# Kernel optimization log

Measured on AMD Instinct MI355X. Metric: run time of the kernel, lower is better.

Reference implementation:

```python
import jax, jax.numpy as jnp
import numpy as np

DIM = 768
NUM_HEADS = 12
HEAD_DIM = DIM // NUM_HEADS
EPS = 1e-6  # flax nn.LayerNorm default


def layer_norm(x, scale, bias):
    # LayerNorm over last axis (head_dim)
    mean = jnp.mean(x, axis=-1, keepdims=True)
    var = jnp.var(x, axis=-1, keepdims=True)
    return (x - mean) * jax.lax.rsqrt(var + EPS) * scale + bias


def setup_inputs() -> dict:
    key = jax.random.key(0)
    k0, = jax.random.split(key, 1)
    B, N = 4, 2048
    QKV = jax.random.normal(k0, (B, N, 3 * DIM), dtype=jnp.float32)
    return {
        "QKV": QKV,
        "q_scale": jnp.ones((HEAD_DIM,), jnp.float32),
        "q_bias": jnp.zeros((HEAD_DIM,), jnp.float32),
        "k_scale": jnp.ones((HEAD_DIM,), jnp.float32),
        "k_bias": jnp.zeros((HEAD_DIM,), jnp.float32),
    }


def reference(QKV, q_scale, q_bias, k_scale, k_bias):
    B, N, C = QKV.shape
    qkv = QKV.reshape(B, N, 3, NUM_HEADS, HEAD_DIM)
    qkv = jnp.transpose(qkv, (2, 0, 3, 1, 4))  # [3, B, H, N, d]
    q, k, v = qkv[0], qkv[1], qkv[2]
    q = layer_norm(q, q_scale, q_bias)
    k = layer_norm(k, k_scale, k_bias)
    attn = jnp.einsum('bhqd,bhkd->bhqk', q, k) * (HEAD_DIM ** -0.5)
    attn = jax.nn.softmax(attn, axis=-1)
    x = jnp.einsum('bhqk,bhkd->bhqd', attn, v)
    return x
```

## Files before the change

### kernel.cpp

```cpp
#include <hip/hip_runtime.h>
#include <math.h>

#define NB   4
#define SEQ  2048
#define NH   12
#define CIN  2304
#define TM   64
#define NCH  (SEQ/TM)
#define TQ   128

typedef _Float16 half8 __attribute__((ext_vector_type(8)));
typedef _Float16 half4 __attribute__((ext_vector_type(4)));
typedef float    f32x4 __attribute__((ext_vector_type(4)));
typedef unsigned int u32;
#define AS1 __attribute__((address_space(1)))
#define AS3 __attribute__((address_space(3)))

#define TILE_B  8192
#define KT_BYTES ((size_t)NB*NH*NCH*TILE_B)
#define WS_FULL  (2*KT_BYTES)

static __device__ __forceinline__ int dec_xcd(int id, int& b, int& h, int& q0) {
    const int xcd = id & 7;
    const int qt  = (id >> 3) & 15;
    const int grp = id >> 7;
    const int bh  = grp * 8 + xcd;
    b = bh / NH; h = bh - b * NH; q0 = qt * TQ;
    return bh;
}

__global__ __launch_bounds__(256, 4)
void preprocess_kernel(const float* __restrict__ QKV,
                       const float* __restrict__ k_scale,
                       const float* __restrict__ k_bias,
                       unsigned char* __restrict__ ws, int writeV)
{
    const int tid = threadIdx.x;
    const int L   = tid & 63;
    const int wv  = tid >> 6;
    const int r4  = L >> 2;
    const int c4  = L & 3;
    const int mc  = blockIdx.x, h = blockIdx.y, b = blockIdx.z;

    unsigned char* Kt = ws + (size_t)((b*NH + h)*NCH + mc) * TILE_B;

    const float4* QKV4 = (const float4*)QKV;
    const int row = wv*16 + r4;
    const size_t base4 = (size_t)(b*SEQ + mc*64 + row) * 576 + h*16 + c4*4;

    {
        float4 x[4];
        #pragma unroll
        for (int i = 0; i < 4; ++i) x[i] = QKV4[base4 + 192 + i];
        float s = 0.f, s2 = 0.f;
        #pragma unroll
        for (int i = 0; i < 4; ++i) {
            s  += x[i].x + x[i].y + x[i].z + x[i].w;
            s2 += x[i].x*x[i].x + x[i].y*x[i].y + x[i].z*x[i].z + x[i].w*x[i].w;
        }
        s  += __shfl_xor(s, 1);  s  += __shfl_xor(s, 2);
        s2 += __shfl_xor(s2, 1); s2 += __shfl_xor(s2, 2);
        float mu = s * 0.015625f;
        float rstd = rsqrtf(s2 * 0.015625f - mu*mu + 1e-6f);
        float nb0 = -mu * rstd;
        half8 h0, h1;
        #pragma unroll
        for (int i = 0; i < 4; ++i) {
            float4 sc = ((const float4*)k_scale)[c4*4 + i];
            float4 bi = ((const float4*)k_bias)[c4*4 + i];
            float e0 = fmaf(x[i].x, rstd, nb0) * sc.x + bi.x;
            float e1 = fmaf(x[i].y, rstd, nb0) * sc.y + bi.y;
            float e2 = fmaf(x[i].z, rstd, nb0) * sc.z + bi.z;
            float e3 = fmaf(x[i].w, rstd, nb0) * sc.w + bi.w;
            if (i < 2) { h0[i*4+0]=(_Float16)e0; h0[i*4+1]=(_Float16)e1; h0[i*4+2]=(_Float16)e2; h0[i*4+3]=(_Float16)e3; }
            else { int j=(i-2)*4; h1[j+0]=(_Float16)e0; h1[j+1]=(_Float16)e1; h1[j+2]=(_Float16)e2; h1[j+3]=(_Float16)e3; }
        }
        *(half8*)(Kt + row*128 + (((2*c4+0) ^ (row & 7)) * 16)) = h0;
        *(half8*)(Kt + row*128 + (((2*c4+1) ^ (row & 7)) * 16)) = h1;
    }

    if (writeV) {
        unsigned char* Vt = ws + KT_BYTES + (size_t)((b*NH + h)*NCH + mc) * TILE_B;
        const float* gv = QKV + (size_t)(b*SEQ + mc*64 + wv*16)*CIN + 1536 + h*64 + L;
        float vvp[16];
        #pragma unroll
        for (int j = 0; j < 16; ++j) vvp[j] = gv[(size_t)j * CIN];
        half8 a0, a1;
        #pragma unroll
        for (int j = 0; j < 8; ++j) { a0[j] = (_Float16)vvp[j]; a1[j] = (_Float16)vvp[j+8]; }
        *(half8*)(Vt + L*128 + (((2*wv+0) ^ (L & 7)) * 16)) = a0;
        *(half8*)(Vt + L*128 + (((2*wv+1) ^ (L & 7)) * 16)) = a1;
    }
}

#define Q_PROLOGUE(QTBASE)                                                        \
    const float SC = 0.125f * 1.44269504088896340736f;                            \
    _Pragma("unroll")                                                             \
    for (int g = 0; g < 2; ++g) {                                                 \
        const int row = wv*32 + g*16 + r4;                                        \
        const size_t base4 = (size_t)(b*SEQ + q0 + row) * 576 + h*16 + c4*4;      \
        float4 x[4];                                                              \
        _Pragma("unroll")                                                         \
        for (int i = 0; i < 4; ++i) x[i] = QKV4[base4 + i];                       \
        float s = 0.f, s2 = 0.f;                                                  \
        _Pragma("unroll")                                                         \
        for (int i = 0; i < 4; ++i) {                                             \
            s  += x[i].x + x[i].y + x[i].z + x[i].w;                              \
            s2 += x[i].x*x[i].x + x[i].y*x[i].y + x[i].z*x[i].z + x[i].w*x[i].w;  \
        }                                                                         \
        s  += __shfl_xor(s, 1);  s  += __shfl_xor(s, 2);                          \
        s2 += __shfl_xor(s2, 1); s2 += __shfl_xor(s2, 2);                         \
        float mu = s * 0.015625f;                                                 \
        float rstd = rsqrtf(s2 * 0.015625f - mu*mu + 1e-6f);                      \
        float nb0 = -mu * rstd;                                                   \
        half8 h0, h1;                                                             \
        _Pragma("unroll")                                                         \
        for (int i = 0; i < 4; ++i) {                                             \
            float4 sc = ((const float4*)q_scale)[c4*4 + i];                       \
            float4 bi = ((const float4*)q_bias)[c4*4 + i];                        \
            float e0 = (fmaf(x[i].x, rstd, nb0) * sc.x + bi.x) * SC;              \
            float e1 = (fmaf(x[i].y, rstd, nb0) * sc.y + bi.y) * SC;              \
            float e2 = (fmaf(x[i].z, rstd, nb0) * sc.z + bi.z) * SC;              \
            float e3 = (fmaf(x[i].w, rstd, nb0) * sc.w + bi.w) * SC;              \
            if (i < 2) { h0[i*4+0]=(_Float16)e0; h0[i*4+1]=(_Float16)e1; h0[i*4+2]=(_Float16)e2; h0[i*4+3]=(_Float16)e3; } \
            else { int j=(i-2)*4; h1[j+0]=(_Float16)e0; h1[j+1]=(_Float16)e1; h1[j+2]=(_Float16)e2; h1[j+3]=(_Float16)e3; } \
        }                                                                         \
        *(half8*)((QTBASE) + row*128 + (((2*c4+0) ^ (r4 & 7)) * 16)) = h0;        \
        *(half8*)((QTBASE) + row*128 + (((2*c4+1) ^ (r4 & 7)) * 16)) = h1;        \
    }                                                                             \
    half8 qf[2][2];                                                               \
    _Pragma("unroll")                                                             \
    for (int s = 0; s < 2; ++s) {                                                 \
        const unsigned char* qrow = (QTBASE) + (wv*32 + s*16 + n16)*128;          \
        _Pragma("unroll")                                                         \
        for (int ks = 0; ks < 2; ++ks)                                            \
            qf[s][ks] = *(const half8*)(qrow + (((quad + 4*ks) ^ sw) * 16));      \
    }

#define CHUNK_COMPUTE(KAB, VTB)                                                   \
    {                                                                             \
        f32x4 sacc[2][4] = {};                                                    \
        _Pragma("unroll")                                                         \
        for (int ks = 0; ks < 2; ++ks) {                                          \
            half8 ak[4];                                                          \
            _Pragma("unroll")                                                     \
            for (int mt = 0; mt < 4; ++mt)                                        \
                ak[mt] = *(const half8*)((KAB) + (16*mt + n16)*128 + (((quad + 4*ks) ^ sw) * 16)); \
            _Pragma("unroll")                                                     \
            for (int s = 0; s < 2; ++s)                                           \
                _Pragma("unroll")                                                 \
                for (int mt = 0; mt < 4; ++mt)                                    \
                    sacc[s][mt] = __builtin_amdgcn_mfma_f32_16x16x32_f16(ak[mt], qf[s][ks], sacc[s][mt], 0, 0, 0); \
        }                                                                         \
        _Pragma("unroll")                                                         \
        for (int s = 0; s < 2; ++s) {                                             \
            float ls = 0.f;                                                       \
            _Pragma("unroll")                                                     \
            for (int mt = 0; mt < 4; ++mt) {                                      \
                float p0 = __builtin_exp2f(sacc[s][mt][0]);                       \
                float p1 = __builtin_exp2f(sacc[s][mt][1]);                       \
                float p2 = __builtin_exp2f(sacc[s][mt][2]);                       \
                float p3 = __builtin_exp2f(sacc[s][mt][3]);                       \
                ls += (p0 + p1) + (p2 + p3);                                      \
                half4 hp; hp[0]=(_Float16)p0; hp[1]=(_Float16)p1; hp[2]=(_Float16)p2; hp[3]=(_Float16)p3; \
                *(half4*)(Pw + s*2048 + n16*128 + (((4*mt + quad) ^ n16) * 8)) = hp; \
            }                                                                     \
            ls += __shfl_xor(ls, 16);                                             \
            ls += __shfl_xor(ls, 32);                                             \
            lsum[s] += ls;                                                        \
        }                                                                         \
        _Pragma("unroll")                                                         \
        for (int ks = 0; ks < 2; ++ks) {                                          \
            half8 av[4];                                                          \
            _Pragma("unroll")                                                     \
            for (int mt = 0; mt < 4; ++mt)                                        \
                av[mt] = *(const half8*)((VTB) + (16*mt + n16)*128 + (((quad + 4*ks) ^ sw) * 16)); \
            _Pragma("unroll")                                                     \
            for (int s = 0; s < 2; ++s) {                                         \
                half4 b0 = *(const half4*)(Pw + s*2048 + n16*128 + (((8*ks + 2*quad + 0) ^ n16) * 8)); \
                half4 b1 = *(const half4*)(Pw + s*2048 + n16*128 + (((8*ks + 2*quad + 1) ^ n16) * 8)); \
                half8 bp;                                                         \
                _Pragma("unroll")                                                 \
                for (int j = 0; j < 4; ++j) { bp[j] = b0[j]; bp[4+j] = b1[j]; }   \
                _Pragma("unroll")                                                 \
                for (int mt = 0; mt < 4; ++mt)                                    \
                    oacc[s][mt] = __builtin_amdgcn_mfma_f32_16x16x32_f16(av[mt], bp, oacc[s][mt], 0, 0, 0); \
            }                                                                     \
        }                                                                         \
    }

#define EPILOGUE()                                                                \
    {                                                                             \
        float4* out4 = (float4*)out;                                              \
        _Pragma("unroll")                                                         \
        for (int s = 0; s < 2; ++s) {                                             \
            float inv = 1.0f / lsum[s];                                           \
            size_t rowb = ((size_t)(b*NH + h)*SEQ + q0 + wv*32 + s*16 + n16) * 16;\
            _Pragma("unroll")                                                     \
            for (int mt = 0; mt < 4; ++mt)                                        \
                out4[rowb + mt*4 + quad] = make_float4(oacc[s][mt][0]*inv, oacc[s][mt][1]*inv, oacc[s][mt][2]*inv, oacc[s][mt][3]*inv); \
        }                                                                         \
    }

#define COMMON_IDS()                                                              \
    const int tid  = threadIdx.x;                                                 \
    const int L    = tid & 63;                                                    \
    const int wv   = tid >> 6;                                                    \
    const int n16  = L & 15;                                                      \
    const int quad = L >> 4;                                                      \
    const int sw   = n16 & 7;                                                     \
    const int r4   = L >> 2;                                                      \
    const int c4   = L & 3;                                                       \
    int b, h, q0; dec_xcd(blockIdx.x, b, h, q0);                                  \
    const float4* QKV4 = (const float4*)QKV;

__global__ __launch_bounds__(256, 3)
void attn_full(const float* __restrict__ QKV,
               const float* __restrict__ q_scale,
               const float* __restrict__ q_bias,
               const unsigned char* __restrict__ ws,
               float* __restrict__ out)
{
    __shared__ __align__(16) unsigned char sm[49152];
    COMMON_IDS()
    unsigned char* Qt = sm + 32768;
    unsigned char* Pw = Qt + wv*4096;

    const unsigned char* Ktiles = ws + (size_t)((b*NH + h)*NCH) * TILE_B;
    const unsigned char* Vtiles = ws + KT_BYTES + (size_t)((b*NH + h)*NCH) * TILE_B;

    #define ISSUE_KV(MC, P)                                                       \
    {                                                                             \
        const unsigned char* kt_ = Ktiles + (size_t)(MC) * TILE_B;                \
        const unsigned char* vt_ = Vtiles + (size_t)(MC) * TILE_B;                \
        unsigned char* lk_ = sm + (P)*16384;                                      \
        unsigned char* lv_ = lk_ + 8192;                                          \
        _Pragma("unroll")                                                         \
        for (int t_ = 0; t_ < 2; ++t_) {                                          \
            int seg_ = wv*2 + t_;                                                 \
            __builtin_amdgcn_global_load_lds((const AS1 u32*)(kt_ + seg_*1024 + L*16), \
                                             (AS3 u32*)(lk_ + seg_*1024), 16, 0, 0);   \
            __builtin_amdgcn_global_load_lds((const AS1 u32*)(vt_ + seg_*1024 + L*16), \
                                             (AS3 u32*)(lv_ + seg_*1024), 16, 0, 0);   \
        }                                                                         \
    }

    ISSUE_KV(0, 0)
    Q_PROLOGUE(Qt)

    f32x4 oacc[2][4] = {};
    float lsum[2] = {0.f, 0.f};

    for (int mc = 0; mc < NCH; ++mc) {
        const int p = mc & 1;
        __syncthreads();
        if (mc + 1 < NCH) ISSUE_KV(mc + 1, p ^ 1)
        const unsigned char* Ka = sm + p*16384;
        const unsigned char* Vt = Ka + 8192;
        CHUNK_COMPUTE(Ka, Vt)
    }
    EPILOGUE()
    #undef ISSUE_KV
}

__global__ __launch_bounds__(256, 3)
void attn_ktile(const float* __restrict__ QKV,
                const float* __restrict__ q_scale,
                const float* __restrict__ q_bias,
                const unsigned char* __restrict__ ws,
                float* __restrict__ out)
{
    __shared__ __align__(16) unsigned char sm[40960];
    COMMON_IDS()
    unsigned char* Vt = sm + 16384;
    unsigned char* Qt = sm + 24576;
    unsigned char* Pw = Qt + wv*4096;

    const unsigned char* Ktiles = ws + (size_t)((b*NH + h)*NCH) * TILE_B;

    #define ISSUE_K(MC, P)                                                        \
    {                                                                             \
        const unsigned char* kt_ = Ktiles + (size_t)(MC) * TILE_B;                \
        unsigned char* lk_ = sm + (P)*8192;                                       \
        _Pragma("unroll")                                                         \
        for (int t_ = 0; t_ < 2; ++t_) {                                          \
            int seg_ = wv*2 + t_;                                                 \
            __builtin_amdgcn_global_load_lds((const AS1 u32*)(kt_ + seg_*1024 + L*16), \
                                             (AS3 u32*)(lk_ + seg_*1024), 16, 0, 0);   \
        }                                                                         \
    }
    float vv[16];
    #define PREFETCH_V(MC)                                                        \
    {                                                                             \
        const float* gv = QKV + (size_t)(b*SEQ + (MC)*64 + wv*16) * CIN + 1536 + h*64 + L; \
        _Pragma("unroll")                                                         \
        for (int j = 0; j < 16; ++j) vv[j] = gv[(size_t)j * CIN];                 \
    }
    #define STAGE_V()                                                             \
    {                                                                             \
        half8 a0, a1;                                                             \
        _Pragma("unroll")                                                         \
        for (int j = 0; j < 8; ++j) { a0[j] = (_Float16)vv[j]; a1[j] = (_Float16)vv[j+8]; } \
        *(half8*)(Vt + L*128 + (((2*wv+0) ^ (L & 7)) * 16)) = a0;                 \
        *(half8*)(Vt + L*128 + (((2*wv+1) ^ (L & 7)) * 16)) = a1;                 \
    }

    PREFETCH_V(0)
    ISSUE_K(0, 0)
    Q_PROLOGUE(Qt)

    f32x4 oacc[2][4] = {};
    float lsum[2] = {0.f, 0.f};

    for (int mc = 0; mc < NCH; ++mc) {
        const int p = mc & 1;
        __syncthreads();
        STAGE_V()
        __syncthreads();
        if (mc + 1 < NCH) { ISSUE_K(mc + 1, p ^ 1) PREFETCH_V(mc + 1) }
        const unsigned char* Ka = sm + p*8192;
        CHUNK_COMPUTE(Ka, Vt)
    }
    EPILOGUE()
    #undef ISSUE_K
    #undef PREFETCH_V
    #undef STAGE_V
}

__global__ __launch_bounds__(256, 3)
void fused_fallback(const float* __restrict__ QKV,
                    const float* __restrict__ q_scale,
                    const float* __restrict__ q_bias,
                    const float* __restrict__ k_scale,
                    const float* __restrict__ k_bias,
                    float* __restrict__ out)
{
    __shared__ __align__(16) unsigned char sm[32768];
    COMMON_IDS()
    unsigned char* Ka = sm;
    unsigned char* Vt = sm + 8192;
    unsigned char* Qt = sm + 16384;
    unsigned char* Pw = Qt + wv*4096;

    float4 ksr[4], kbr[4];
    #pragma unroll
    for (int i = 0; i < 4; ++i) {
        ksr[i] = ((const float4*)k_scale)[c4 * 4 + i];
        kbr[i] = ((const float4*)k_bias)[c4 * 4 + i];
    }
    float4 kx[4];
    float  vv[16];
    #define PREFETCH(MC)                                                          \
    {                                                                             \
        const size_t kb4 = (size_t)(b*SEQ + (MC)*64 + wv*16 + r4) * 576 + 192 + h*16 + c4*4; \
        _Pragma("unroll")                                                         \
        for (int i = 0; i < 4; ++i) kx[i] = QKV4[kb4 + i];                        \
        const float* gv = QKV + (size_t)(b*SEQ + (MC)*64 + wv*16) * CIN + 1536 + h*64 + L; \
        _Pragma("unroll")                                                         \
        for (int j = 0; j < 16; ++j) vv[j] = gv[(size_t)j * CIN];                 \
    }
    #define STAGE_KV()                                                            \
    {                                                                             \
        const int row = wv*16 + r4;                                               \
        float s = 0.f, s2 = 0.f;                                                  \
        _Pragma("unroll")                                                         \
        for (int i = 0; i < 4; ++i) {                                             \
            s  += kx[i].x + kx[i].y + kx[i].z + kx[i].w;                          \
            s2 += kx[i].x*kx[i].x + kx[i].y*kx[i].y + kx[i].z*kx[i].z + kx[i].w*kx[i].w; \
        }                                                                         \
        s  += __shfl_xor(s, 1);  s  += __shfl_xor(s, 2);                          \
        s2 += __shfl_xor(s2, 1); s2 += __shfl_xor(s2, 2);                         \
        float mu = s * 0.015625f;                                                 \
        float rstd = rsqrtf(s2 * 0.015625f - mu*mu + 1e-6f);                      \
        float nb0 = -mu * rstd;                                                   \
        half8 h0, h1;                                                             \
        _Pragma("unroll")                                                         \
        for (int i = 0; i < 4; ++i) {                                             \
            float e0 = fmaf(kx[i].x, rstd, nb0) * ksr[i].x + kbr[i].x;            \
            float e1 = fmaf(kx[i].y, rstd, nb0) * ksr[i].y + kbr[i].y;            \
            float e2 = fmaf(kx[i].z, rstd, nb0) * ksr[i].z + kbr[i].z;            \
            float e3 = fmaf(kx[i].w, rstd, nb0) * ksr[i].w + kbr[i].w;            \
            if (i < 2) { h0[i*4+0]=(_Float16)e0; h0[i*4+1]=(_Float16)e1; h0[i*4+2]=(_Float16)e2; h0[i*4+3]=(_Float16)e3; } \
            else { int j=(i-2)*4; h1[j+0]=(_Float16)e0; h1[j+1]=(_Float16)e1; h1[j+2]=(_Float16)e2; h1[j+3]=(_Float16)e3; } \
        }                                                                         \
        *(half8*)(Ka + row*128 + (((2*c4+0) ^ (row & 7)) * 16)) = h0;             \
        *(half8*)(Ka + row*128 + (((2*c4+1) ^ (row & 7)) * 16)) = h1;             \
        half8 a0, a1;                                                             \
        _Pragma("unroll")                                                         \
        for (int j = 0; j < 8; ++j) { a0[j] = (_Float16)vv[j]; a1[j] = (_Float16)vv[j+8]; } \
        *(half8*)(Vt + L*128 + (((2*wv+0) ^ (L & 7)) * 16)) = a0;                 \
        *(half8*)(Vt + L*128 + (((2*wv+1) ^ (L & 7)) * 16)) = a1;                 \
    }

    PREFETCH(0)
    Q_PROLOGUE(Qt)

    f32x4 oacc[2][4] = {};
    float lsum[2] = {0.f, 0.f};

    for (int mc = 0; mc < NCH; ++mc) {
        __syncthreads();
        STAGE_KV()
        __syncthreads();
        if (mc + 1 < NCH) PREFETCH(mc + 1)
        CHUNK_COMPUTE(Ka, Vt)
    }
    EPILOGUE()
    #undef PREFETCH
    #undef STAGE_KV
}

extern "C" void kernel_launch(void* const* d_in, const int* in_sizes, int n_in,
                              void* d_out, int out_size, void* d_ws, size_t ws_size,
                              hipStream_t stream) {
    const float* QKV     = (const float*)d_in[0];
    const float* q_scale = (const float*)d_in[1];
    const float* q_bias  = (const float*)d_in[2];
    const float* k_scale = (const float*)d_in[3];
    const float* k_bias  = (const float*)d_in[4];
    float* out = (float*)d_out;
    unsigned char* ws = (unsigned char*)d_ws;

    const dim3 agrid(NB * NH * (SEQ / TQ));
    if (ws_size >= WS_FULL) {
        preprocess_kernel<<<dim3(NCH, NH, NB), 256, 0, stream>>>(QKV, k_scale, k_bias, ws, 1);
        attn_full<<<agrid, 256, 0, stream>>>(QKV, q_scale, q_bias, ws, out);
    } else if (ws_size >= KT_BYTES) {
        preprocess_kernel<<<dim3(NCH, NH, NB), 256, 0, stream>>>(QKV, k_scale, k_bias, ws, 0);
        attn_ktile<<<agrid, 256, 0, stream>>>(QKV, q_scale, q_bias, ws, out);
    } else {
        fused_fallback<<<agrid, 256, 0, stream>>>(QKV, q_scale, q_bias, k_scale, k_bias, out);
    }
}
```

Baseline: 212.9 us.

## Read K/V tiles directly from global memory instead of staging through LDS

The main attention kernel stops double-buffering preprocessed K and V tiles into shared memory with async global-to-LDS loads and barriers. Each wave now reads its MFMA operands straight from the global workspace, which relies on L2/L1 caching and cuts shared memory from 48KB to 16KB per block. It also hoists all V operand loads ahead of the softmax section so their latency overlaps the exp work. The tradeoff is that every wave reissues global loads for the same tiles, and the loop loses the explicit prefetch overlap, with more register pressure from the hoisted V fragments.

```diff
diff --git a/kernel.cpp b/kernel.cpp
--- a/kernel.cpp
+++ b/kernel.cpp
@@ -152,6 +152,13 @@
                 for (int mt = 0; mt < 4; ++mt)                                    \
                     sacc[s][mt] = __builtin_amdgcn_mfma_f32_16x16x32_f16(ak[mt], qf[s][ks], sacc[s][mt], 0, 0, 0); \
         }                                                                         \
+                \
+        half8 av[2][4];                                                           \
+        _Pragma("unroll")                                                         \
+        for (int ks = 0; ks < 2; ++ks)                                            \
+            _Pragma("unroll")                                                     \
+            for (int mt = 0; mt < 4; ++mt)                                        \
+                av[ks][mt] = *(const half8*)((VTB) + (16*mt + n16)*128 + (((quad + 4*ks) ^ sw) * 16)); \
         _Pragma("unroll")                                                         \
         for (int s = 0; s < 2; ++s) {                                             \
             float ls = 0.f;                                                       \
@@ -171,10 +178,6 @@
         }                                                                         \
         _Pragma("unroll")                                                         \
         for (int ks = 0; ks < 2; ++ks) {                                          \
-            half8 av[4];                                                          \
-            _Pragma("unroll")                                                     \
-            for (int mt = 0; mt < 4; ++mt)                                        \
-                av[mt] = *(const half8*)((VTB) + (16*mt + n16)*128 + (((quad + 4*ks) ^ sw) * 16)); \
             _Pragma("unroll")                                                     \
             for (int s = 0; s < 2; ++s) {                                         \
                 half4 b0 = *(const half4*)(Pw + s*2048 + n16*128 + (((8*ks + 2*quad + 0) ^ n16) * 8)); \
@@ -184,7 +187,7 @@
                 for (int j = 0; j < 4; ++j) { bp[j] = b0[j]; bp[4+j] = b1[j]; }   \
                 _Pragma("unroll")                                                 \
                 for (int mt = 0; mt < 4; ++mt)                                    \
-                    oacc[s][mt] = __builtin_amdgcn_mfma_f32_16x16x32_f16(av[mt], bp, oacc[s][mt], 0, 0, 0); \
+                    oacc[s][mt] = __builtin_amdgcn_mfma_f32_16x16x32_f16(av[ks][mt], bp, oacc[s][mt], 0, 0, 0); \
             }                                                                     \
         }                                                                         \
     }
@@ -215,52 +218,29 @@
     const float4* QKV4 = (const float4*)QKV;
 
 __global__ __launch_bounds__(256, 3)
-void attn_full(const float* __restrict__ QKV,
-               const float* __restrict__ q_scale,
-               const float* __restrict__ q_bias,
-               const unsigned char* __restrict__ ws,
-               float* __restrict__ out)
+void attn_direct(const float* __restrict__ QKV,
+                 const float* __restrict__ q_scale,
+                 const float* __restrict__ q_bias,
+                 const unsigned char* __restrict__ ws,
+                 float* __restrict__ out)
 {
-    __shared__ __align__(16) unsigned char sm[49152];
+    __shared__ __align__(16) unsigned char sm[16384];
     COMMON_IDS()
-    unsigned char* Qt = sm + 32768;
+    unsigned char* Qt = sm;
     unsigned char* Pw = Qt + wv*4096;
 
-    const unsigned char* Ktiles = ws + (size_t)((b*NH + h)*NCH) * TILE_B;
-    const unsigned char* Vtiles = ws + KT_BYTES + (size_t)((b*NH + h)*NCH) * TILE_B;
-
-    #define ISSUE_KV(MC, P)                                                       \
-    {                                                                             \
-        const unsigned char* kt_ = Ktiles + (size_t)(MC) * TILE_B;                \
-        const unsigned char* vt_ = Vtiles + (size_t)(MC) * TILE_B;                \
-        unsigned char* lk_ = sm + (P)*16384;                                      \
-        unsigned char* lv_ = lk_ + 8192;                                          \
-        _Pragma("unroll")                                                         \
-        for (int t_ = 0; t_ < 2; ++t_) {                                          \
-            int seg_ = wv*2 + t_;                                                 \
-            __builtin_amdgcn_global_load_lds((const AS1 u32*)(kt_ + seg_*1024 + L*16), \
-                                             (AS3 u32*)(lk_ + seg_*1024), 16, 0, 0);   \
-            __builtin_amdgcn_global_load_lds((const AS1 u32*)(vt_ + seg_*1024 + L*16), \
-                                             (AS3 u32*)(lv_ + seg_*1024), 16, 0, 0);   \
-        }                                                                         \
-    }
-
-    ISSUE_KV(0, 0)
+    const unsigned char* Kt = ws + (size_t)((b*NH + h)*NCH) * TILE_B;
+    const unsigned char* Vt = ws + KT_BYTES + (size_t)((b*NH + h)*NCH) * TILE_B;
+
     Q_PROLOGUE(Qt)
 
     f32x4 oacc[2][4] = {};
     float lsum[2] = {0.f, 0.f};
 
-    for (int mc = 0; mc < NCH; ++mc) {
-        const int p = mc & 1;
-        __syncthreads();
-        if (mc + 1 < NCH) ISSUE_KV(mc + 1, p ^ 1)
-        const unsigned char* Ka = sm + p*16384;
-        const unsigned char* Vt = Ka + 8192;
-        CHUNK_COMPUTE(Ka, Vt)
+    for (int mc = 0; mc < NCH; ++mc, Kt += TILE_B, Vt += TILE_B) {
+        CHUNK_COMPUTE(Kt, Vt)
     }
     EPILOGUE()
-    #undef ISSUE_KV
 }
 
 __global__ __launch_bounds__(256, 3)
@@ -424,7 +404,7 @@
     const dim3 agrid(NB * NH * (SEQ / TQ));
     if (ws_size >= WS_FULL) {
         preprocess_kernel<<<dim3(NCH, NH, NB), 256, 0, stream>>>(QKV, k_scale, k_bias, ws, 1);
-        attn_full<<<agrid, 256, 0, stream>>>(QKV, q_scale, q_bias, ws, out);
+        attn_direct<<<agrid, 256, 0, stream>>>(QKV, q_scale, q_bias, ws, out);
     } else if (ws_size >= KT_BYTES) {
         preprocess_kernel<<<dim3(NCH, NH, NB), 256, 0, stream>>>(QKV, k_scale, k_bias, ws, 0);
         attn_ktile<<<agrid, 256, 0, stream>>>(QKV, q_scale, q_bias, ws, out);
```

After: 233.2 us. +9.6%, slower.
